# Performance work log

Measured on AMD Instinct MI355X. Metric: run time of the kernel, lower is better.

Reference implementation:

```python
import jax, jax.numpy as jnp
import numpy as np

TOPK = 13
ALPHA = 1.0
BETA = 6.0
EPS = 1e-9


def setup_inputs() -> dict:
    key = jax.random.key(0)
    ks = jax.random.split(key, 8)
    B, A, C, M = 32, 8400, 80, 64
    IMG = 640.0
    pred_scores = jax.random.uniform(ks[0], (B, A, C), jnp.float32)  # sigmoid-like scores in [0,1]
    anchor_points = jax.random.uniform(ks[1], (A, 2), jnp.float32, 0.0, IMG)
    off = jax.random.uniform(ks[2], (B, A, 4), jnp.float32, 4.0, 64.0)
    # valid x1y1x2y2 predicted boxes around anchor centers
    pred_bboxes = jnp.concatenate([anchor_points[None] - off[..., :2],
                                   anchor_points[None] + off[..., 2:]], axis=-1)
    gt_labels = jax.random.randint(ks[3], (B, M, 1), 0, C, jnp.int32)
    cxy = jax.random.uniform(ks[4], (B, M, 2), jnp.float32, 20.0, IMG - 20.0)
    wh = jax.random.uniform(ks[5], (B, M, 2), jnp.float32, 8.0, 200.0)
    gt_bboxes = jnp.concatenate([jnp.clip(cxy - 0.5 * wh, 0.0, IMG),
                                 jnp.clip(cxy + 0.5 * wh, 0.0, IMG)], axis=-1)
    nvalid = jax.random.randint(ks[6], (B, 1), 8, M + 1)
    pad_gt_mask = (jnp.arange(M)[None, :] < nvalid).astype(jnp.float32)[..., None]  # [B,M,1] prefix mask
    return {"pred_scores": pred_scores, "pred_bboxes": pred_bboxes,
            "anchor_points": anchor_points, "gt_labels": gt_labels,
            "gt_bboxes": gt_bboxes, "pad_gt_mask": pad_gt_mask, "bg_index": 80}


def reference(pred_scores, pred_bboxes, anchor_points, gt_labels, gt_bboxes, pad_gt_mask, bg_index):
    B, A, C = pred_scores.shape
    M = gt_bboxes.shape[1]

    # ---- pairwise IoU: gt [B,M,1,4] vs pred [B,1,A,4] -> [B,M,A] ----
    b1 = gt_bboxes[:, :, None, :]
    b2 = pred_bboxes[:, None, :, :]
    x1y1 = jnp.maximum(b1[..., :2], b2[..., :2])
    x2y2 = jnp.minimum(b1[..., 2:], b2[..., 2:])
    overlap = jnp.prod(jnp.clip(x2y2 - x1y1, 0.0, None), axis=-1)
    area1 = jnp.prod(jnp.clip(b1[..., 2:] - b1[..., :2], 0.0, None), axis=-1)
    area2 = jnp.prod(jnp.clip(b2[..., 2:] - b2[..., :2], 0.0, None), axis=-1)
    ious = overlap / (area1 + area2 - overlap + EPS)  # [B,M,A]

    # ---- classification score of each anchor at each GT's label -> [B,M,A] ----
    scores_t = jnp.transpose(pred_scores, (0, 2, 1))  # [B,C,A]
    bbox_cls_scores = jnp.take_along_axis(scores_t, gt_labels, axis=1)  # idx [B,M,1] -> [B,M,A]

    align = (bbox_cls_scores ** ALPHA) * (ious ** BETA)  # alignment metric [B,M,A]

    # ---- anchors-inside-gt mask [B,M,A] ----
    px = anchor_points[None, None, :, 0]
    py = anchor_points[None, None, :, 1]
    xmin = gt_bboxes[:, :, None, 0]; ymin = gt_bboxes[:, :, None, 1]
    xmax = gt_bboxes[:, :, None, 2]; ymax = gt_bboxes[:, :, None, 3]
    d = jnp.minimum(jnp.minimum(px - xmin, py - ymin), jnp.minimum(xmax - px, ymax - py))
    is_in_gts = (d > EPS).astype(align.dtype)

    # ---- top-k gating along anchors ----
    metrics = align * is_in_gts
    _, topk_idxs = jax.lax.top_k(metrics, TOPK)  # [B,M,TOPK]
    bi = jnp.arange(B)[:, None, None]
    mi = jnp.arange(M)[None, :, None]
    is_in_topk = jnp.zeros_like(metrics).at[bi, mi, topk_idxs].add(1.0)
    is_in_topk = is_in_topk * pad_gt_mask  # topk_mask = pad_gt_mask

    mask_positive = is_in_topk * is_in_gts * pad_gt_mask  # [B,M,A]
    mask_positive_sum = mask_positive.sum(axis=-2)  # [B,A]

    # ---- resolve anchors claimed by multiple GTs via max-IoU ----
    multi = (mask_positive_sum[:, None, :] > 1)  # [B,1,A] broadcasts over M
    max_iou_idx = jnp.argmax(ious, axis=-2)  # [B,A]
    is_max_iou = (jnp.arange(M)[None, :, None] == max_iou_idx[:, None, :]).astype(ious.dtype)
    mask_positive = jnp.where(multi, is_max_iou, mask_positive)
    mask_positive_sum = mask_positive.sum(axis=-2)

    # ---- assemble assignments ----
    assigned_gt_index = jnp.argmax(mask_positive, axis=-2)  # [B,A]
    assigned_labels = jnp.take_along_axis(gt_labels[..., 0], assigned_gt_index, axis=1)  # [B,A]
    assigned_labels = jnp.where(mask_positive_sum > 0, assigned_labels, bg_index)
    assigned_bboxes = jnp.take_along_axis(gt_bboxes, assigned_gt_index[..., None], axis=1)  # [B,A,4]

    one_hot = jax.nn.one_hot(assigned_labels, C + 1, dtype=align.dtype)
    keep = jnp.array([i for i in range(C + 1) if i != bg_index], dtype=jnp.int32)
    assigned_scores = one_hot[..., keep]  # [B,A,C]

    # ---- rescale alignment metrics into soft targets ----
    am = align * mask_positive
    max_metrics = am.max(axis=-1, keepdims=True)  # [B,M,1]
    max_ious = (ious * mask_positive).max(axis=-1, keepdims=True)
    am = am / (max_metrics + EPS) * max_ious
    assigned_scores = assigned_scores * am.max(axis=-2)[..., None]

    return assigned_labels, assigned_bboxes, assigned_scores
```

## Files before the change

kernel.cpp:

```cpp
#include <hip/hip_runtime.h>
#include <stdint.h>

#define BB 32
#define AA 8400
#define CC 80
#define MM 64
#define KTOP 13
#define FEPS 1e-9f
#define CAND_CAP 1024
#define CNT_STRIDE 16

typedef unsigned long long u64;

__device__ __forceinline__ float iou_fn(float gx1, float gy1, float gx2, float gy2,
                                        float px1, float py1, float px2, float py2) {
    float ix1 = fmaxf(gx1, px1), iy1 = fmaxf(gy1, py1);
    float ix2 = fminf(gx2, px2), iy2 = fminf(gy2, py2);
    float ov = fmaxf(ix2 - ix1, 0.0f) * fmaxf(iy2 - iy1, 0.0f);
    float a1 = fmaxf(gx2 - gx1, 0.0f) * fmaxf(gy2 - gy1, 0.0f);
    float a2 = fmaxf(px2 - px1, 0.0f) * fmaxf(py2 - py1, 0.0f);
    return ov / (a1 + a2 - ov + FEPS);
}

__global__ __launch_bounds__(256) void pairgen_kernel(
    const float* __restrict__ pred_scores, const float* __restrict__ pred_bboxes,
    const float* __restrict__ anchors, const int* __restrict__ gt_labels,
    const float* __restrict__ gt_bboxes, const float* __restrict__ pad_mask,
    int* __restrict__ cnt, u64* __restrict__ cand)
{
    __shared__ float4 gtb_s[MM];
    __shared__ int    gtl_s[MM];
    __shared__ u64    valid_s;
    int b = blockIdx.y;
    int t = threadIdx.x;
    if (t < MM) {
        gtb_s[t] = ((const float4*)gt_bboxes)[b * MM + t];
        gtl_s[t] = gt_labels[b * MM + t];
        bool v = pad_mask[b * MM + t] != 0.0f;
        u64 bal = __ballot(v);
        if (t == 0) valid_s = bal;
    }
    __syncthreads();
    int a = blockIdx.x * 256 + t;
    if (a >= AA) return;
    float2 xy = *(const float2*)(anchors + a * 2);
    float4 p = ((const float4*)pred_bboxes)[(size_t)b * AA + a];
    const float4* gg = (const float4*)gt_bboxes + b * MM;
    u64 mask = 0;
    #pragma unroll 8
    for (int m = 0; m < MM; ++m) {
        float4 g = gg[m];
        float d = fminf(fminf(xy.x - g.x, xy.y - g.y), fminf(g.z - xy.x, g.w - xy.y));
        mask |= ((u64)(d > FEPS)) << m;
    }
    mask &= valid_s;
    if (!mask) return;
    float parea = (p.z - p.x) * (p.w - p.y);
    const float* psa = pred_scores + ((size_t)b * AA + a) * CC;
    unsigned ia = (unsigned)(AA - a);
    while (mask) {
        int m = __ffsll(mask) - 1;
        mask &= mask - 1;
        float4 g = gtb_s[m];
        float ix1 = fmaxf(g.x, p.x), iy1 = fmaxf(g.y, p.y);
        float ix2 = fminf(g.z, p.z), iy2 = fminf(g.w, p.w);
        float ov = fmaxf(ix2 - ix1, 0.0f) * fmaxf(iy2 - iy1, 0.0f);
        float garea = (g.z - g.x) * (g.w - g.y);
        float iou = ov / (garea + parea - ov + FEPS);
        float s = psa[gtl_s[m]];
        float i2 = iou * iou;
        float met = s * (i2 * i2 * i2);
        if (met > 0.0f) {
            int bm = b * MM + m;
            int slot = atomicAdd(&cnt[bm * CNT_STRIDE], 1);
            if (slot < CAND_CAP)
                cand[(size_t)bm * CAND_CAP + slot] =
                    ((u64)__float_as_uint(met) << 32) | ia;
        }
    }
}

__global__ __launch_bounds__(256) void select_scatter_kernel(
    const int* __restrict__ cnt, const u64* __restrict__ cand,
    u64* __restrict__ mask64)
{
    int bm = blockIdx.x;
    int n = min(cnt[bm * CNT_STRIDE], CAND_CAP);
    int rounds = min(n, KTOP);
    if (rounds == 0) return;
    int b = bm >> 6, m = bm & 63;
    int t = threadIdx.x;
    __shared__ u64 rv[2][4];
    u64 c[4];
    #pragma unroll
    for (int j = 0; j < 4; ++j) {
        int i = t + j * 256;
        c[j] = (i < n) ? cand[(size_t)bm * CAND_CAP + i] : 0;
    }
    int lane = t & 63, wv = t >> 6;
    for (int k = 0; k < rounds; ++k) {
        u64 bk = c[0];
        #pragma unroll
        for (int j = 1; j < 4; ++j) bk = (c[j] > bk) ? c[j] : bk;
        #pragma unroll
        for (int off = 32; off > 0; off >>= 1) {
            u64 ok = __shfl_xor(bk, off);
            bk = (ok > bk) ? ok : bk;
        }
        if (lane == 0) rv[k & 1][wv] = bk;
        __syncthreads();
        u64 wk = rv[k & 1][0];
        #pragma unroll
        for (int w = 1; w < 4; ++w) wk = (rv[k & 1][w] > wk) ? rv[k & 1][w] : wk;
        #pragma unroll
        for (int j = 0; j < 4; ++j) if (c[j] == wk) c[j] = 0;
        if (t == 0) {
            int a = AA - (int)(wk & 0xffffffffULL);
            atomicOr(&mask64[(size_t)b * AA + a], 1ull << m);
        }
    }
}

__global__ __launch_bounds__(256) void resolve_kernel(
    const float* __restrict__ pred_scores, const float* __restrict__ pred_bboxes,
    const int* __restrict__ gt_labels, const float* __restrict__ gt_bboxes,
    const int* __restrict__ bg_ptr,
    const u64* __restrict__ mask64,
    float* __restrict__ out_labels, float* __restrict__ out_bboxes,
    int* __restrict__ assigned_m, float* __restrict__ assigned_align,
    unsigned int* __restrict__ maxmet, unsigned int* __restrict__ maxiou)
{
    __shared__ float4 gtb_s[MM];
    __shared__ int    gtl_s[MM];
    int b = blockIdx.y;
    int t = threadIdx.x;
    if (t < MM) {
        gtb_s[t] = ((const float4*)gt_bboxes)[b * MM + t];
        gtl_s[t] = gt_labels[b * MM + t];
    }
    __syncthreads();
    int a = blockIdx.x * 256 + t;
    if (a >= AA) return;
    size_t ga = (size_t)b * AA + a;
    u64 mask = mask64[ga];
    int cnt = __popcll(mask);
    float4 p = ((const float4*)pred_bboxes)[ga];
    int mstar = -1;
    if (cnt == 1) {
        mstar = __ffsll(mask) - 1;
    } else if (cnt > 1) {
        float best = -1.0f; int bi = 0;
        for (int m = 0; m < MM; ++m) {
            float4 g = gtb_s[m];
            float iou = iou_fn(g.x, g.y, g.z, g.w, p.x, p.y, p.z, p.w);
            if (iou > best) { best = iou; bi = m; }
        }
        mstar = bi;
    }
    assigned_m[ga] = mstar;
    int bidx = (mstar >= 0) ? mstar : 0;
    float4 g = gtb_s[bidx];
    ((float4*)out_bboxes)[ga] = g;
    out_labels[ga] = (mstar >= 0) ? (float)gtl_s[mstar] : (float)(*bg_ptr);
    if (mstar >= 0) {
        float iou = iou_fn(g.x, g.y, g.z, g.w, p.x, p.y, p.z, p.w);
        float s = pred_scores[ga * CC + gtl_s[mstar]];
        float i2 = iou * iou;
        float al = s * (i2 * i2 * i2);
        assigned_align[ga] = al;
        atomicMax(&maxmet[b * MM + mstar], __float_as_uint(al));
        atomicMax(&maxiou[b * MM + mstar], __float_as_uint(iou));
    }
}

__global__ __launch_bounds__(256) void scores_kernel(
    const int* __restrict__ gt_labels,
    const int* __restrict__ assigned_m, const float* __restrict__ assigned_align,
    const unsigned int* __restrict__ maxmet, const unsigned int* __restrict__ maxiou,
    float* __restrict__ out_scores)
{
    int t = blockIdx.x * blockDim.x + threadIdx.x;
    if (t >= BB * AA * (CC / 4)) return;
    int anchor = t / (CC / 4); int j = t % (CC / 4);
    int m = assigned_m[anchor];
    float4 v = make_float4(0.0f, 0.0f, 0.0f, 0.0f);
    if (m >= 0) {
        int b = anchor / AA;
        int label = gt_labels[b * MM + m];
        int base = j * 4;
        if (label >= base && label < base + 4) {
            float mm = __uint_as_float(maxmet[b * MM + m]);
            float mi = __uint_as_float(maxiou[b * MM + m]);
            float scale = assigned_align[anchor] / (mm + FEPS) * mi;
            ((float*)&v)[label - base] = scale;
        }
    }
    *(float4*)(out_scores + (size_t)t * 4) = v;
}

extern "C" void kernel_launch(void* const* d_in, const int* in_sizes, int n_in,
                              void* d_out, int out_size, void* d_ws, size_t ws_size,
                              hipStream_t stream) {
    const float* pred_scores = (const float*)d_in[0];
    const float* pred_bboxes = (const float*)d_in[1];
    const float* anchors     = (const float*)d_in[2];
    const int*   gt_labels   = (const int*)d_in[3];
    const float* gt_bboxes   = (const float*)d_in[4];
    const float* pad_mask    = (const float*)d_in[5];
    const int*   bg_ptr      = (const int*)d_in[6];

    char* ws = (char*)d_ws;
    size_t off = 0;
    u64* mask64 = (u64*)(ws + off);
    off += (size_t)BB * AA * sizeof(u64);
    int* cnt = (int*)(ws + off);
    off += (size_t)BB * MM * CNT_STRIDE * sizeof(int);
    unsigned int* maxmet = (unsigned int*)(ws + off);
    off += (size_t)BB * MM * sizeof(unsigned int);
    unsigned int* maxiou = (unsigned int*)(ws + off);
    off += (size_t)BB * MM * sizeof(unsigned int);
    size_t zero_bytes = off;
    u64* cand = (u64*)(ws + off);
    off += (size_t)BB * MM * CAND_CAP * sizeof(u64);
    int* assigned_m = (int*)(ws + off);
    off += (size_t)BB * AA * sizeof(int);
    float* assigned_align = (float*)(ws + off);
    off += (size_t)BB * AA * sizeof(float);

    hipMemsetAsync(ws, 0, zero_bytes, stream);

    float* out = (float*)d_out;
    float* out_labels = out;
    float* out_bboxes = out + (size_t)BB * AA;
    float* out_scores = out + (size_t)BB * AA * 5;

    dim3 gridA((AA + 255) / 256, BB);
    pairgen_kernel<<<gridA, 256, 0, stream>>>(
        pred_scores, pred_bboxes, anchors, gt_labels, gt_bboxes, pad_mask,
        cnt, cand);

    select_scatter_kernel<<<BB * MM, 256, 0, stream>>>(cnt, cand, mask64);

    resolve_kernel<<<gridA, 256, 0, stream>>>(
        pred_scores, pred_bboxes, gt_labels, gt_bboxes, bg_ptr, mask64,
        out_labels, out_bboxes, assigned_m, assigned_align, maxmet, maxiou);

    int n4 = BB * AA * (CC / 4);
    scores_kernel<<<(n4 + 255) / 256, 256, 0, stream>>>(
        gt_labels, assigned_m, assigned_align, maxmet, maxiou, out_scores);
}
```

Before: 264.4 us.

## Fuse four assignment kernels into one cooperative kernel with grid syncs

Replaces the four launches (pair generation, top-k select/scatter, resolve, score fill) with a single cooperative kernel of 1024 blocks. Grid-wide syncs separate the phases, and each block keeps its batch's GT boxes in shared memory across phases. The goal is to remove inter-kernel launch gaps and tail effects. In exchange, occupancy is capped at a fixed grid size, and a fallback to the original kernels runs if the cooperative launch fails.

```diff
diff --git a/kernel.cpp b/kernel.cpp
--- a/kernel.cpp
+++ b/kernel.cpp
@@ -1,5 +1,8 @@
 #include <hip/hip_runtime.h>
+#include <hip/hip_cooperative_groups.h>
 #include <stdint.h>
+
+namespace cg = cooperative_groups;
 
 #define BB 32
 #define AA 8400
@@ -10,6 +13,11 @@
 #define CAND_CAP 1024
 #define CNT_STRIDE 16
 
+#define CBLK 1024
+#define CHB (CBLK / BB)
+#define ABLK ((AA + CHB - 1) / CHB)
+#define NQUAD (BB * AA * (CC / 4))
+
 typedef unsigned long long u64;
 
 __device__ __forceinline__ float iou_fn(float gx1, float gy1, float gx2, float gy2,
@@ -21,6 +29,179 @@
     float a2 = fmaxf(px2 - px1, 0.0f) * fmaxf(py2 - py1, 0.0f);
     return ov / (a1 + a2 - ov + FEPS);
 }
+
+__global__ __launch_bounds__(256, 4) void fused_kernel(
+    const float* __restrict__ pred_scores, const float* __restrict__ pred_bboxes,
+    const float* __restrict__ anchors, const int* __restrict__ gt_labels,
+    const float* __restrict__ gt_bboxes, const float* __restrict__ pad_mask,
+    const int* __restrict__ bg_ptr,
+    int* __restrict__ cnt, u64* __restrict__ cand,
+    u64* __restrict__ mask64,
+    unsigned int* __restrict__ maxmet, unsigned int* __restrict__ maxiou,
+    int* __restrict__ assigned_m, float* __restrict__ assigned_align,
+    float* __restrict__ out_labels, float* __restrict__ out_bboxes,
+    float* __restrict__ out_scores)
+{
+    __shared__ float4 gtb_s[MM];
+    __shared__ int    gtl_s[MM];
+    __shared__ u64    valid_s;
+    __shared__ u64    cv_rv[4];
+
+    cg::grid_group grid = cg::this_grid();
+    int blk = blockIdx.x;
+    int t = threadIdx.x;
+    int b = blk / CHB, chunk = blk % CHB;
+
+    if (t < MM) {
+        gtb_s[t] = ((const float4*)gt_bboxes)[b * MM + t];
+        gtl_s[t] = gt_labels[b * MM + t];
+        bool v = pad_mask[b * MM + t] != 0.0f;
+        u64 bal = __ballot(v);
+        if (t == 0) valid_s = bal;
+    }
+    __syncthreads();
+    for (int i = t; i < ABLK; i += 256) {
+        int a = chunk * ABLK + i;
+        if (a >= AA) break;
+        float2 xy = *(const float2*)(anchors + a * 2);
+        float4 p = ((const float4*)pred_bboxes)[(size_t)b * AA + a];
+        const float4* gg = (const float4*)gt_bboxes + b * MM;
+        u64 mask = 0;
+        #pragma unroll 8
+        for (int m = 0; m < MM; ++m) {
+            float4 g = gg[m];
+            float d = fminf(fminf(xy.x - g.x, xy.y - g.y),
+                            fminf(g.z - xy.x, g.w - xy.y));
+            mask |= ((u64)(d > FEPS)) << m;
+        }
+        mask &= valid_s;
+        float parea = (p.z - p.x) * (p.w - p.y);
+        const float* psa = pred_scores + ((size_t)b * AA + a) * CC;
+        unsigned ia = (unsigned)(AA - a);
+        while (mask) {
+            int m = __ffsll(mask) - 1;
+            mask &= mask - 1;
+            float4 g = gtb_s[m];
+            float ix1 = fmaxf(g.x, p.x), iy1 = fmaxf(g.y, p.y);
+            float ix2 = fminf(g.z, p.z), iy2 = fminf(g.w, p.w);
+            float ov = fmaxf(ix2 - ix1, 0.0f) * fmaxf(iy2 - iy1, 0.0f);
+            float garea = (g.z - g.x) * (g.w - g.y);
+            float iou = ov / (garea + parea - ov + FEPS);
+            float s = psa[gtl_s[m]];
+            float i2 = iou * iou;
+            float met = s * (i2 * i2 * i2);
+            if (met > 0.0f) {
+                int bm = b * MM + m;
+                int slot = atomicAdd(&cnt[bm * CNT_STRIDE], 1);
+                if (slot < CAND_CAP)
+                    cand[(size_t)bm * CAND_CAP + slot] =
+                        ((u64)__float_as_uint(met) << 32) | ia;
+            }
+        }
+    }
+    __threadfence();
+    grid.sync();
+
+    {
+        int lane = t & 63, wv = t >> 6;
+        for (int r = 0; r < 2; ++r) {
+            int bm = blk * 2 + r;
+            int n = min(cnt[bm * CNT_STRIDE], CAND_CAP);
+            int rounds = min(n, KTOP);
+            if (rounds > 0) {
+                int rb = bm >> 6, rm = bm & 63;
+                u64 c[4];
+                #pragma unroll
+                for (int j = 0; j < 4; ++j) {
+                    int i = t + j * 256;
+                    c[j] = (i < n) ? cand[(size_t)bm * CAND_CAP + i] : 0;
+                }
+                for (int k = 0; k < rounds; ++k) {
+                    u64 bk = c[0];
+                    #pragma unroll
+                    for (int j = 1; j < 4; ++j) bk = (c[j] > bk) ? c[j] : bk;
+                    #pragma unroll
+                    for (int off = 32; off > 0; off >>= 1) {
+                        u64 ok = __shfl_xor(bk, off);
+                        bk = (ok > bk) ? ok : bk;
+                    }
+                    if (lane == 0) cv_rv[wv] = bk;
+                    __syncthreads();
+                    u64 wk = cv_rv[0];
+                    #pragma unroll
+                    for (int w = 1; w < 4; ++w) wk = (cv_rv[w] > wk) ? cv_rv[w] : wk;
+                    #pragma unroll
+                    for (int j = 0; j < 4; ++j) if (c[j] == wk) c[j] = 0;
+                    if (t == 0) {
+                        int a = AA - (int)(wk & 0xffffffffULL);
+                        atomicOr(&mask64[(size_t)rb * AA + a], 1ull << rm);
+                    }
+                    __syncthreads();
+                }
+            }
+            __syncthreads();
+        }
+    }
+    __threadfence();
+    grid.sync();
+
+    for (int i = t; i < ABLK; i += 256) {
+        int a = chunk * ABLK + i;
+        if (a >= AA) break;
+        size_t ga = (size_t)b * AA + a;
+        u64 mask = mask64[ga];
+        int pc = __popcll(mask);
+        float4 p = ((const float4*)pred_bboxes)[ga];
+        int mstar = -1;
+        if (pc == 1) {
+            mstar = __ffsll(mask) - 1;
+        } else if (pc > 1) {
+            float best = -1.0f; int bi = 0;
+            for (int m = 0; m < MM; ++m) {
+                float4 g = gtb_s[m];
+                float iou = iou_fn(g.x, g.y, g.z, g.w, p.x, p.y, p.z, p.w);
+                if (iou > best) { best = iou; bi = m; }
+            }
+            mstar = bi;
+        }
+        assigned_m[ga] = mstar;
+        int bidx = (mstar >= 0) ? mstar : 0;
+        float4 g = gtb_s[bidx];
+        ((float4*)out_bboxes)[ga] = g;
+        out_labels[ga] = (mstar >= 0) ? (float)gtl_s[mstar] : (float)(*bg_ptr);
+        if (mstar >= 0) {
+            float iou = iou_fn(g.x, g.y, g.z, g.w, p.x, p.y, p.z, p.w);
+            float s = pred_scores[ga * CC + gtl_s[mstar]];
+            float i2 = iou * iou;
+            float al = s * (i2 * i2 * i2);
+            assigned_align[ga] = al;
+            atomicMax(&maxmet[b * MM + mstar], __float_as_uint(al));
+            atomicMax(&maxiou[b * MM + mstar], __float_as_uint(iou));
+        }
+    }
+    __threadfence();
+    grid.sync();
+
+    for (int q = blk * 256 + t; q < NQUAD; q += CBLK * 256) {
+        int anchor = q / (CC / 4);
+        int j = q - anchor * (CC / 4);
+        int m = assigned_m[anchor];
+        float4 v = make_float4(0.0f, 0.0f, 0.0f, 0.0f);
+        if (m >= 0) {
+            int qb = anchor / AA;
+            int label = gt_labels[qb * MM + m];
+            int base = j * 4;
+            if (label >= base && label < base + 4) {
+                float mm = __uint_as_float(maxmet[qb * MM + m]);
+                float mi = __uint_as_float(maxiou[qb * MM + m]);
+                float scale = assigned_align[anchor] / (mm + FEPS) * mi;
+                ((float*)&v)[label - base] = scale;
+            }
+        }
+        *(float4*)(out_scores + (size_t)q * 4) = v;
+    }
+}
+
 
 __global__ __launch_bounds__(256) void pairgen_kernel(
     const float* __restrict__ pred_scores, const float* __restrict__ pred_bboxes,
@@ -143,12 +324,12 @@
     if (a >= AA) return;
     size_t ga = (size_t)b * AA + a;
     u64 mask = mask64[ga];
-    int cnt = __popcll(mask);
+    int pc = __popcll(mask);
     float4 p = ((const float4*)pred_bboxes)[ga];
     int mstar = -1;
-    if (cnt == 1) {
+    if (pc == 1) {
         mstar = __ffsll(mask) - 1;
-    } else if (cnt > 1) {
+    } else if (pc > 1) {
         float best = -1.0f; int bi = 0;
         for (int m = 0; m < MM; ++m) {
             float4 g = gtb_s[m];
@@ -180,7 +361,7 @@
     float* __restrict__ out_scores)
 {
     int t = blockIdx.x * blockDim.x + threadIdx.x;
-    if (t >= BB * AA * (CC / 4)) return;
+    if (t >= NQUAD) return;
     int anchor = t / (CC / 4); int j = t % (CC / 4);
     int m = assigned_m[anchor];
     float4 v = make_float4(0.0f, 0.0f, 0.0f, 0.0f);
@@ -234,18 +415,27 @@
     float* out_bboxes = out + (size_t)BB * AA;
     float* out_scores = out + (size_t)BB * AA * 5;
 
-    dim3 gridA((AA + 255) / 256, BB);
-    pairgen_kernel<<<gridA, 256, 0, stream>>>(
-        pred_scores, pred_bboxes, anchors, gt_labels, gt_bboxes, pad_mask,
-        cnt, cand);
-
-    select_scatter_kernel<<<BB * MM, 256, 0, stream>>>(cnt, cand, mask64);
-
-    resolve_kernel<<<gridA, 256, 0, stream>>>(
-        pred_scores, pred_bboxes, gt_labels, gt_bboxes, bg_ptr, mask64,
-        out_labels, out_bboxes, assigned_m, assigned_align, maxmet, maxiou);
-
-    int n4 = BB * AA * (CC / 4);
-    scores_kernel<<<(n4 + 255) / 256, 256, 0, stream>>>(
-        gt_labels, assigned_m, assigned_align, maxmet, maxiou, out_scores);
-}
+    void* args[] = {
+        (void*)&pred_scores, (void*)&pred_bboxes, (void*)&anchors,
+        (void*)&gt_labels, (void*)&gt_bboxes, (void*)&pad_mask, (void*)&bg_ptr,
+        (void*)&cnt, (void*)&cand, (void*)&mask64, (void*)&maxmet, (void*)&maxiou,
+        (void*)&assigned_m, (void*)&assigned_align,
+        (void*)&out_labels, (void*)&out_bboxes, (void*)&out_scores
+    };
+    hipError_t cerr = hipLaunchCooperativeKernel((void*)fused_kernel,
+                                                 dim3(CBLK), dim3(256),
+                                                 args, 0, stream);
+    if (cerr != hipSuccess) {
+        (void)hipGetLastError();
+        dim3 gridA((AA + 255) / 256, BB);
+        pairgen_kernel<<<gridA, 256, 0, stream>>>(
+            pred_scores, pred_bboxes, anchors, gt_labels, gt_bboxes, pad_mask,
+            cnt, cand);
+        select_scatter_kernel<<<BB * MM, 256, 0, stream>>>(cnt, cand, mask64);
+        resolve_kernel<<<gridA, 256, 0, stream>>>(
+            pred_scores, pred_bboxes, gt_labels, gt_bboxes, bg_ptr, mask64,
+            out_labels, out_bboxes, assigned_m, assigned_align, maxmet, maxiou);
+        scores_kernel<<<(NQUAD + 255) / 256, 256, 0, stream>>>(
+            gt_labels, assigned_m, assigned_align, maxmet, maxiou, out_scores);
+    }
+}
```

Result: slower. 821.2 us (+210.6%).

## Zero score rows in resolve and scatter positives via sparse fixup list

Applied to the files above, without the earlier changes.

The dense scores kernel, which read assigned_m for every anchor-class chunk, is replaced. The resolve kernel now zero-fills each anchor's score row and appends positive anchors to a compact list via an atomic counter, and a small fixup kernel writes only those positive entries. Clearing mask64 moves from the memset into pairgen, which shrinks the memset. The cost is a global atomic counter contended by all positives, and per-thread strided 320-byte row writes in resolve that may coalesce worse than the old fully coalesced float4 writes.

```diff
diff --git a/kernel.cpp b/kernel.cpp
--- a/kernel.cpp
+++ b/kernel.cpp
@@ -9,6 +9,7 @@
 #define FEPS 1e-9f
 #define CAND_CAP 1024
 #define CNT_STRIDE 16
+#define PLIST_CAP (BB * MM * KTOP)
 
 typedef unsigned long long u64;
 
@@ -26,7 +27,7 @@
     const float* __restrict__ pred_scores, const float* __restrict__ pred_bboxes,
     const float* __restrict__ anchors, const int* __restrict__ gt_labels,
     const float* __restrict__ gt_bboxes, const float* __restrict__ pad_mask,
-    int* __restrict__ cnt, u64* __restrict__ cand)
+    int* __restrict__ cnt, u64* __restrict__ cand, u64* __restrict__ mask64)
 {
     __shared__ float4 gtb_s[MM];
     __shared__ int    gtl_s[MM];
@@ -43,6 +44,7 @@
     __syncthreads();
     int a = blockIdx.x * 256 + t;
     if (a >= AA) return;
+    mask64[(size_t)b * AA + a] = 0ull;
     float2 xy = *(const float2*)(anchors + a * 2);
     float4 p = ((const float4*)pred_bboxes)[(size_t)b * AA + a];
     const float4* gg = (const float4*)gt_bboxes + b * MM;
@@ -127,8 +129,10 @@
     const int* __restrict__ bg_ptr,
     const u64* __restrict__ mask64,
     float* __restrict__ out_labels, float* __restrict__ out_bboxes,
-    int* __restrict__ assigned_m, float* __restrict__ assigned_align,
-    unsigned int* __restrict__ maxmet, unsigned int* __restrict__ maxiou)
+    float* __restrict__ out_scores,
+    float* __restrict__ assigned_align,
+    unsigned int* __restrict__ maxmet, unsigned int* __restrict__ maxiou,
+    int* __restrict__ pcnt, int2* __restrict__ plist)
 {
     __shared__ float4 gtb_s[MM];
     __shared__ int    gtl_s[MM];
@@ -143,12 +147,12 @@
     if (a >= AA) return;
     size_t ga = (size_t)b * AA + a;
     u64 mask = mask64[ga];
-    int cnt = __popcll(mask);
+    int pc = __popcll(mask);
     float4 p = ((const float4*)pred_bboxes)[ga];
     int mstar = -1;
-    if (cnt == 1) {
+    if (pc == 1) {
         mstar = __ffsll(mask) - 1;
-    } else if (cnt > 1) {
+    } else if (pc > 1) {
         float best = -1.0f; int bi = 0;
         for (int m = 0; m < MM; ++m) {
             float4 g = gtb_s[m];
@@ -157,7 +161,10 @@
         }
         mstar = bi;
     }
-    assigned_m[ga] = mstar;
+    float4 z = make_float4(0.0f, 0.0f, 0.0f, 0.0f);
+    float4* srow = (float4*)(out_scores + ga * CC);
+    #pragma unroll
+    for (int j = 0; j < CC / 4; ++j) srow[j] = z;
     int bidx = (mstar >= 0) ? mstar : 0;
     float4 g = gtb_s[bidx];
     ((float4*)out_bboxes)[ga] = g;
@@ -170,32 +177,29 @@
         assigned_align[ga] = al;
         atomicMax(&maxmet[b * MM + mstar], __float_as_uint(al));
         atomicMax(&maxiou[b * MM + mstar], __float_as_uint(iou));
-    }
-}
-
-__global__ __launch_bounds__(256) void scores_kernel(
+        int idx = atomicAdd(pcnt, 1);
+        plist[idx] = make_int2((int)ga, mstar);
+    }
+}
+
+__global__ __launch_bounds__(256) void fixup_kernel(
     const int* __restrict__ gt_labels,
-    const int* __restrict__ assigned_m, const float* __restrict__ assigned_align,
+    const int* __restrict__ pcnt, const int2* __restrict__ plist,
+    const float* __restrict__ assigned_align,
     const unsigned int* __restrict__ maxmet, const unsigned int* __restrict__ maxiou,
     float* __restrict__ out_scores)
 {
-    int t = blockIdx.x * blockDim.x + threadIdx.x;
-    if (t >= BB * AA * (CC / 4)) return;
-    int anchor = t / (CC / 4); int j = t % (CC / 4);
-    int m = assigned_m[anchor];
-    float4 v = make_float4(0.0f, 0.0f, 0.0f, 0.0f);
-    if (m >= 0) {
-        int b = anchor / AA;
-        int label = gt_labels[b * MM + m];
-        int base = j * 4;
-        if (label >= base && label < base + 4) {
-            float mm = __uint_as_float(maxmet[b * MM + m]);
-            float mi = __uint_as_float(maxiou[b * MM + m]);
-            float scale = assigned_align[anchor] / (mm + FEPS) * mi;
-            ((float*)&v)[label - base] = scale;
-        }
-    }
-    *(float4*)(out_scores + (size_t)t * 4) = v;
+    int i = blockIdx.x * blockDim.x + threadIdx.x;
+    if (i >= *pcnt) return;
+    int2 e = plist[i];
+    size_t ga = (size_t)e.x;
+    int m = e.y;
+    int b = (int)(ga / AA);
+    int label = gt_labels[b * MM + m];
+    float mm = __uint_as_float(maxmet[b * MM + m]);
+    float mi = __uint_as_float(maxiou[b * MM + m]);
+    float scale = assigned_align[ga] / (mm + FEPS) * mi;
+    out_scores[ga * CC + label] = scale;
 }
 
 extern "C" void kernel_launch(void* const* d_in, const int* in_sizes, int n_in,
@@ -211,21 +215,23 @@
 
     char* ws = (char*)d_ws;
     size_t off = 0;
-    u64* mask64 = (u64*)(ws + off);
-    off += (size_t)BB * AA * sizeof(u64);
     int* cnt = (int*)(ws + off);
     off += (size_t)BB * MM * CNT_STRIDE * sizeof(int);
     unsigned int* maxmet = (unsigned int*)(ws + off);
     off += (size_t)BB * MM * sizeof(unsigned int);
     unsigned int* maxiou = (unsigned int*)(ws + off);
     off += (size_t)BB * MM * sizeof(unsigned int);
+    int* pcnt = (int*)(ws + off);
+    off += 16;
     size_t zero_bytes = off;
+    u64* mask64 = (u64*)(ws + off);
+    off += (size_t)BB * AA * sizeof(u64);
     u64* cand = (u64*)(ws + off);
     off += (size_t)BB * MM * CAND_CAP * sizeof(u64);
-    int* assigned_m = (int*)(ws + off);
-    off += (size_t)BB * AA * sizeof(int);
     float* assigned_align = (float*)(ws + off);
     off += (size_t)BB * AA * sizeof(float);
+    int2* plist = (int2*)(ws + off);
+    off += (size_t)PLIST_CAP * sizeof(int2);
 
     hipMemsetAsync(ws, 0, zero_bytes, stream);
 
@@ -237,15 +243,15 @@
     dim3 gridA((AA + 255) / 256, BB);
     pairgen_kernel<<<gridA, 256, 0, stream>>>(
         pred_scores, pred_bboxes, anchors, gt_labels, gt_bboxes, pad_mask,
-        cnt, cand);
+        cnt, cand, mask64);
 
     select_scatter_kernel<<<BB * MM, 256, 0, stream>>>(cnt, cand, mask64);
 
     resolve_kernel<<<gridA, 256, 0, stream>>>(
         pred_scores, pred_bboxes, gt_labels, gt_bboxes, bg_ptr, mask64,
-        out_labels, out_bboxes, assigned_m, assigned_align, maxmet, maxiou);
-
-    int n4 = BB * AA * (CC / 4);
-    scores_kernel<<<(n4 + 255) / 256, 256, 0, stream>>>(
-        gt_labels, assigned_m, assigned_align, maxmet, maxiou, out_scores);
-}
+        out_labels, out_bboxes, out_scores, assigned_align,
+        maxmet, maxiou, pcnt, plist);
+
+    fixup_kernel<<<(PLIST_CAP + 255) / 256, 256, 0, stream>>>(
+        gt_labels, pcnt, plist, assigned_align, maxmet, maxiou, out_scores);
+}
```

Result: no change. 267.0 us (+1.0%).
